# Performance work log

Measured on AMD Instinct MI355X. Metric: run time of the kernel, lower is better.

The kernel has to match this reference:

```python
import jax, jax.numpy as jnp
import numpy as np

D_MODEL = 2048
NUM_HEADS = 16
D_K = D_MODEL // NUM_HEADS
LORA_R = 8
LORA_ALPHA = 16
SCALING = LORA_ALPHA / LORA_R  # 2.0
B, S = 2, 2048


def setup_inputs() -> dict:
    key = jax.random.key(0)
    ks = jax.random.split(key, 17)
    s = 1.0 / np.sqrt(D_MODEL)
    d = {"x": jax.random.normal(ks[0], (B, S, D_MODEL), jnp.float32)}
    i = 1
    for name in ("q", "k", "v", "o"):
        d[f"W{name}"] = jax.random.uniform(ks[i], (D_MODEL, D_MODEL), jnp.float32, -s, s); i += 1
        d[f"b{name}"] = jax.random.uniform(ks[i], (D_MODEL,), jnp.float32, -s, s); i += 1
        d[f"A{name}"] = jax.random.uniform(ks[i], (LORA_R, D_MODEL), jnp.float32, -s, s); i += 1
        # lora_B is zero-initialized in the module, but use small random so grads flow meaningfully
        d[f"B{name}"] = jax.random.normal(ks[i], (D_MODEL, LORA_R), jnp.float32) * 0.01; i += 1
    return d


def _lora_linear(x, W, b, A, Bm):
    # F.linear(x, W, b) + (x @ A.T @ B.T) * scaling
    return x @ W.T + b + ((x @ A.T) @ Bm.T) * SCALING


def reference(x, Wq, bq, Aq, Bq, Wk, bk, Ak, Bk, Wv, bv, Av, Bv, Wo, bo, Ao, Bo):
    batch = x.shape[0]
    q = _lora_linear(x, Wq, bq, Aq, Bq)
    k = _lora_linear(x, Wk, bk, Ak, Bk)
    v = _lora_linear(x, Wv, bv, Av, Bv)
    # [B, S, H, Dk] -> [B, H, S, Dk]
    q = q.reshape(batch, -1, NUM_HEADS, D_K).transpose(0, 2, 1, 3)
    k = k.reshape(batch, -1, NUM_HEADS, D_K).transpose(0, 2, 1, 3)
    v = v.reshape(batch, -1, NUM_HEADS, D_K).transpose(0, 2, 1, 3)
    scores = jnp.einsum("bhqd,bhkd->bhqk", q, k) / jnp.sqrt(jnp.float32(D_K))
    attn = jax.nn.softmax(scores, axis=-1)
    context = jnp.einsum("bhqk,bhkd->bhqd", attn, v)
    context = context.transpose(0, 2, 1, 3).reshape(batch, -1, D_MODEL)
    return _lora_linear(context, Wo, bo, Ao, Bo)
```

## Files before the change

### kernel.cpp

```cpp
#include <hip/hip_runtime.h>
#include <stdint.h>

typedef unsigned short u16;
typedef unsigned int   u32;
typedef __bf16  bf16x8 __attribute__((ext_vector_type(8)));
typedef float   f32x4  __attribute__((ext_vector_type(4)));

#define LORA_SCALE 2.0f
#define QSCALE 0.08838834764831845f
#define LOG2E  1.4426950408889634f
#define RESCALE_THR 8.0f

__device__ __forceinline__ u16 f2bf(float f){
  u32 u = __builtin_bit_cast(u32, f);
  u32 r = (u + 0x7fffu + ((u >> 16) & 1u)) >> 16;
  return (u16)r;
}
__device__ __forceinline__ float bf2f(u16 v){
  return __builtin_bit_cast(float, ((u32)v) << 16);
}
__device__ __forceinline__ u32 cvt_pk_bf16(float lo, float hi){
  u32 d;
  asm("v_cvt_pk_bf16_f32 %0, %1, %2" : "=v"(d) : "v"(lo), "v"(hi));
  return d;
}

typedef __attribute__((address_space(3))) u32 lds_u32_t;
typedef __attribute__((address_space(1))) const u32 g_u32_t;

__device__ __forceinline__ void gload16(const void* g, void* l){
  __builtin_amdgcn_global_load_lds((g_u32_t*)(unsigned long long)g,
                                   (lds_u32_t*)(u32)(unsigned long long)l,
                                   16, 0, 0);
}

__global__ __launch_bounds__(256) void cvt_w4(const float* __restrict__ W0,
    const float* __restrict__ W1, const float* __restrict__ W2,
    const float* __restrict__ W3, u16* __restrict__ wqkv, u16* __restrict__ wo){
  int sel = blockIdx.x >> 11;
  int inner = blockIdx.x & 2047;
  const float* src = sel==0 ? W0 : sel==1 ? W1 : sel==2 ? W2 : W3;
  u16* dst = sel<3 ? (wqkv + (size_t)sel*4194304) : wo;
  int i = (inner*256 + threadIdx.x) * 8;
  float4 a = *(const float4*)(src + i);
  float4 b = *(const float4*)(src + i + 4);
  u16 o[8] = {f2bf(a.x),f2bf(a.y),f2bf(a.z),f2bf(a.w),
              f2bf(b.x),f2bf(b.y),f2bf(b.z),f2bf(b.w)};
  *(uint4*)(dst + i) = *(const uint4*)o;
}

__global__ __launch_bounds__(256) void lora_x_fused(const float* __restrict__ x,
    const float* __restrict__ A0, const float* __restrict__ A1, const float* __restrict__ A2,
    float* __restrict__ xout, u16* __restrict__ xbf){
  int w = threadIdx.x >> 6, lane = threadIdx.x & 63;
  int m = blockIdx.x * 4 + w;
  float acc[3][8];
  #pragma unroll
  for (int g=0; g<3; ++g)
    #pragma unroll
    for (int r=0; r<8; ++r) acc[g][r] = 0.f;
  const float* As[3] = {A0, A1, A2};
  #pragma unroll 1
  for (int it=0; it<8; ++it){
    int k = it*256 + lane*4;
    float4 xv = *(const float4*)(x + (size_t)m*2048 + k);
    u16 o[4] = {f2bf(xv.x), f2bf(xv.y), f2bf(xv.z), f2bf(xv.w)};
    *(uint2*)(xbf + (size_t)m*2048 + k) = *(const uint2*)o;
    #pragma unroll
    for (int g=0; g<3; ++g){
      const float* Ag = As[g];
      #pragma unroll
      for (int r=0; r<8; ++r){
        float4 av = *(const float4*)(Ag + r*2048 + k);
        acc[g][r] += xv.x*av.x + xv.y*av.y + xv.z*av.z + xv.w*av.w;
      }
    }
  }
  #pragma unroll
  for (int g=0; g<3; ++g)
    #pragma unroll
    for (int r=0; r<8; ++r){
      float v = acc[g][r];
      #pragma unroll
      for (int off=32; off; off>>=1) v += __shfl_xor(v, off);
      if (lane == 0) xout[g*32768 + m*8 + r] = v;
    }
}

__global__ __launch_bounds__(256) void lora_xa_bf16(const u16* __restrict__ xin,
    const float* __restrict__ A0, float* __restrict__ xout){
  int w = threadIdx.x >> 6, lane = threadIdx.x & 63;
  int m = blockIdx.x * 4 + w;
  float acc[8];
  #pragma unroll
  for (int r=0; r<8; ++r) acc[r] = 0.f;
  #pragma unroll 1
  for (int it=0; it<8; ++it){
    int k = it*256 + lane*4;
    ushort4 u = *(const ushort4*)(xin + (size_t)m*2048 + k);
    float4 xv = {bf2f(u.x), bf2f(u.y), bf2f(u.z), bf2f(u.w)};
    #pragma unroll
    for (int r=0; r<8; ++r){
      float4 av = *(const float4*)(A0 + r*2048 + k);
      acc[r] += xv.x*av.x + xv.y*av.y + xv.z*av.z + xv.w*av.w;
    }
  }
  #pragma unroll
  for (int r=0; r<8; ++r){
    float v = acc[r];
    #pragma unroll
    for (int off=32; off; off>>=1) v += __shfl_xor(v, off);
    if (lane == 0) xout[m*8 + r] = v;
  }
}

__device__ __forceinline__ void gemm_core_pipe(
    const u16* __restrict__ Arow, const u16* __restrict__ Wrow,
    u16* lds, int tid, f32x4 acc[4][4]){
  const int Kd = 2048, NT = 64;
  int w = tid >> 6, lane = tid & 63;
  int l15 = lane & 15, l4 = lane >> 4;
  int wm = w >> 1, wn = w & 1;
  int d0 = tid*16,        r0 = d0>>6, c0 = ((((d0>>4)&3) ^ ((r0>>1)&3))<<3);
  int d1 = 4096 + tid*16, r1 = d1>>6, c1 = ((((d1>>4)&3) ^ ((r1>>1)&3))<<3);

  auto STAGE = [&](int t, int pb){
    int kt = t*32;
    char* LA = (char*)lds + pb*16384;
    char* LB = LA + 8192;
    gload16(Arow + (size_t)r0*Kd + kt + c0, LA + w*1024);
    gload16(Wrow + (size_t)r0*Kd + kt + c0, LB + w*1024);
    gload16(Arow + (size_t)r1*Kd + kt + c1, LA + 4096 + w*1024);
    gload16(Wrow + (size_t)r1*Kd + kt + c1, LB + 4096 + w*1024);
  };

  STAGE(0,0); STAGE(1,1);
  asm volatile("s_waitcnt vmcnt(4)" ::: "memory");
  __builtin_amdgcn_s_barrier();

  int pc = 0, pn = 2;
  #pragma unroll 1
  for (int t=0; t<NT; ++t){
    if (t < NT-2) STAGE(t+2, pn);
    const u16* LA = lds + pc*8192;
    const u16* LB = LA + 4096;
    bf16x8 af[4], bfv[4];
    #pragma unroll
    for (int mi=0; mi<4; mi++){
      int r = wm*64 + mi*16 + l15;
      af[mi] = *(const bf16x8*)(LA + r*32 + ((l4 ^ ((r>>1)&3))<<3));
    }
    #pragma unroll
    for (int ni=0; ni<4; ni++){
      int r = wn*64 + ni*16 + l15;
      bfv[ni] = *(const bf16x8*)(LB + r*32 + ((l4 ^ ((r>>1)&3))<<3));
    }
    __builtin_amdgcn_s_setprio(1);
    #pragma unroll
    for (int mi=0; mi<4; mi++)
      #pragma unroll
      for (int ni=0; ni<4; ni++)
        acc[mi][ni] = __builtin_amdgcn_mfma_f32_16x16x32_bf16(af[mi], bfv[ni], acc[mi][ni], 0, 0, 0);
    __builtin_amdgcn_s_setprio(0);
    if (t < NT-2){
      asm volatile("s_waitcnt vmcnt(4)" ::: "memory");
      __builtin_amdgcn_s_barrier();
    } else if (t == NT-2){
      asm volatile("s_waitcnt vmcnt(0)" ::: "memory");
      __builtin_amdgcn_s_barrier();
    }
    pc = pc==2 ? 0 : pc+1;
    pn = pn==2 ? 0 : pn+1;
  }
}

__global__ __launch_bounds__(256, 3) void gemm_qkv(
    const u16* __restrict__ A, const u16* __restrict__ W,
    const float* __restrict__ bq, const float* __restrict__ bk, const float* __restrict__ bv,
    const float* __restrict__ lBq, const float* __restrict__ lBk, const float* __restrict__ lBv,
    const float* __restrict__ xa, u16* __restrict__ Qb, u16* __restrict__ Kb, u16* __restrict__ Vb){
  const int Kd = 2048;
  __shared__ u16 lds3[3*8192];
  int tid = threadIdx.x, lane = tid & 63;
  int l15 = lane & 15, l4 = lane >> 4;
  int w = tid >> 6, wm = w >> 1, wn = w & 1;
  int n0g = blockIdx.x * 128, m0 = blockIdx.y * 128;
  int which = blockIdx.x >> 4;
  int n0 = n0g & 2047;
  const float* bias = which==0 ? bq : which==1 ? bk : bv;
  const float* lB   = which==0 ? lBq : which==1 ? lBk : lBv;
  const float* xs   = xa + which*32768;
  u16* outp         = which==0 ? Qb : which==1 ? Kb : Vb;
  int swz = (which <= 1);
  float oscale = (which == 0) ? QSCALE*LOG2E : 1.0f;
  f32x4 acc[4][4];
  #pragma unroll
  for (int mi=0; mi<4; mi++)
    #pragma unroll
    for (int ni=0; ni<4; ni++) acc[mi][ni] = (f32x4){0.f,0.f,0.f,0.f};

  gemm_core_pipe(A + (size_t)m0*Kd, W + (size_t)n0g*Kd, lds3, tid, acc);

  float bvv[4]; float4 lb0[4], lb1[4];
  #pragma unroll
  for (int ni=0; ni<4; ni++){
    int col = n0 + wn*64 + ni*16 + l15;
    bvv[ni] = bias[col];
    lb0[ni] = *(const float4*)(lB + col*8);
    lb1[ni] = *(const float4*)(lB + col*8 + 4);
  }
  #pragma unroll
  for (int mi=0; mi<4; mi++)
    #pragma unroll
    for (int j=0; j<4; j++){
      int r = m0 + wm*64 + mi*16 + l4*4 + j;
      float4 xv0 = *(const float4*)(xs + (size_t)r*8);
      float4 xv1 = *(const float4*)(xs + (size_t)r*8 + 4);
      #pragma unroll
      for (int ni=0; ni<4; ni++){
        int col = n0 + wn*64 + ni*16 + l15;
        float v = acc[mi][ni][j] + bvv[ni] + LORA_SCALE * (
            xv0.x*lb0[ni].x + xv0.y*lb0[ni].y + xv0.z*lb0[ni].z + xv0.w*lb0[ni].w +
            xv1.x*lb1[ni].x + xv1.y*lb1[ni].y + xv1.z*lb1[ni].z + xv1.w*lb1[ni].w);
        v *= oscale;
        int cs = swz ? (col ^ ((r & 7) << 3)) : col;
        outp[(size_t)r*2048 + cs] = f2bf(v);
      }
    }
}

__global__ __launch_bounds__(256, 3) void gemm_o(
    const u16* __restrict__ A, const u16* __restrict__ W,
    const float* __restrict__ bias, const float* __restrict__ lB,
    const float* __restrict__ xa, float* __restrict__ outp){
  const int Kd = 2048, Nd = 2048;
  __shared__ u16 lds3[3*8192];
  int tid = threadIdx.x, lane = tid & 63;
  int l15 = lane & 15, l4 = lane >> 4;
  int w = tid >> 6, wm = w >> 1, wn = w & 1;
  int n0 = blockIdx.x * 128, m0 = blockIdx.y * 128;
  f32x4 acc[4][4];
  #pragma unroll
  for (int mi=0; mi<4; mi++)
    #pragma unroll
    for (int ni=0; ni<4; ni++) acc[mi][ni] = (f32x4){0.f,0.f,0.f,0.f};

  gemm_core_pipe(A + (size_t)m0*Kd, W + (size_t)n0*Kd, lds3, tid, acc);

  float bv[4]; float4 lb0[4], lb1[4];
  #pragma unroll
  for (int ni=0; ni<4; ni++){
    int col = n0 + wn*64 + ni*16 + l15;
    bv[ni] = bias[col];
    lb0[ni] = *(const float4*)(lB + col*8);
    lb1[ni] = *(const float4*)(lB + col*8 + 4);
  }
  #pragma unroll
  for (int mi=0; mi<4; mi++)
    #pragma unroll
    for (int j=0; j<4; j++){
      int r = m0 + wm*64 + mi*16 + l4*4 + j;
      float4 xv0 = *(const float4*)(xa + (size_t)r*8);
      float4 xv1 = *(const float4*)(xa + (size_t)r*8 + 4);
      #pragma unroll
      for (int ni=0; ni<4; ni++){
        int col = n0 + wn*64 + ni*16 + l15;
        float v = acc[mi][ni][j] + bv[ni] + LORA_SCALE * (
            xv0.x*lb0[ni].x + xv0.y*lb0[ni].y + xv0.z*lb0[ni].z + xv0.w*lb0[ni].w +
            xv1.x*lb1[ni].x + xv1.y*lb1[ni].y + xv1.z*lb1[ni].z + xv1.w*lb1[ni].w);
        outp[(size_t)r*Nd + col] = v;
      }
    }
}

__global__ __launch_bounds__(256) void transpose_v(const u16* __restrict__ V,
                                                   u16* __restrict__ Vt){
  __shared__ u16 tile[64*80];
  int tid = threadIdx.x;
  int f0 = blockIdx.x * 64, m0 = blockIdx.y * 64;
  int i = tid >> 2, j0 = (tid & 3) * 16;
  #pragma unroll
  for (int kk=0; kk<16; kk+=8){
    uint4 u = *(const uint4*)(V + (size_t)(m0 + i)*2048 + f0 + j0 + kk);
    *(uint4*)(tile + i*80 + j0 + kk) = u;
  }
  __syncthreads();
  int j = tid >> 2, i0 = (tid & 3) * 16;
  int b = m0 >> 11, s0 = m0 & 2047;
  int h = f0 >> 7, d = (f0 & 127) + j;
  int c = (d & 7) << 3;
  size_t obase = ((size_t)((b*16 + h)*128 + d)) * 2048 + s0;
  #pragma unroll
  for (int kk=0; kk<16; kk+=8){
    u16 v8[8];
    #pragma unroll
    for (int u2=0; u2<8; ++u2) v8[u2] = tile[(i0+kk+u2)*80 + j];
    *(uint4*)(Vt + obase + ((i0+kk) ^ c)) = *(const uint4*)v8;
  }
}

__global__ __launch_bounds__(256, 2) void attn_kernel(
    const u16* __restrict__ Q, const u16* __restrict__ K,
    const u16* __restrict__ Vt, u16* __restrict__ ctx){
  __shared__ u16 buf[2][16384];
  __shared__ u16 Psh[4*32*64];
  int tid = threadIdx.x, w = tid >> 6, lane = tid & 63;
  int l15 = lane & 15, l4 = lane >> 4;
  int lin = blockIdx.x;
  int virt = (lin & 7) * 64 + (lin >> 3);
  int qt = virt & 15, bh = virt >> 4;
  int b = bh >> 4, h = bh & 15;
  const u16* Qg = Q + (size_t)(b*2048 + qt*128) * 2048 + h*128;
  const u16* Kg = K + (size_t)(b*2048) * 2048 + h*128;
  const u16* Vg = Vt + (size_t)bh * 128 * 2048;

  #pragma unroll
  for (int i=0; i<8; ++i){
    int e = (i*256 + tid) * 8;
    int r = e >> 7, cc = e & 127;
    gload16(Qg + (size_t)r*2048 + cc, (char*)buf[1] + i*4096 + w*1024);
  }
  #pragma unroll
  for (int i=0; i<4; ++i){
    int e = (i*256 + tid) * 8;
    int r = e >> 7, cc = e & 127;
    gload16(Kg + (size_t)r*2048 + cc, (char*)buf[0] + i*4096 + w*1024);
    int dd = e >> 6, c2 = e & 63;
    gload16(Vg + (size_t)dd*2048 + c2, (char*)buf[0] + 16384 + i*4096 + w*1024);
  }
  __syncthreads();

  bf16x8 qf[2][4];
  #pragma unroll
  for (int mi=0; mi<2; mi++){
    int r = w*32 + mi*16 + l15;
    #pragma unroll
    for (int kb=0; kb<4; kb++){
      int cc = (kb*32 + l4*8) ^ ((r & 7) << 3);
      qf[mi][kb] = *(const bf16x8*)(buf[1] + r*128 + cc);
    }
  }
  __syncthreads();

  f32x4 ctxa[2][8];
  #pragma unroll
  for (int mi=0; mi<2; mi++)
    #pragma unroll
    for (int nd=0; nd<8; nd++) ctxa[mi][nd] = (f32x4){0.f,0.f,0.f,0.f};
  float mrun[2] = {-3.0e38f, -3.0e38f};
  float lrun[2] = {0.f, 0.f};

  char* PwB = (char*)(Psh + w * (32*64));
  int psw = (l15 & 7) << 4;

  for (int t = 0; t < 32; ++t){
    int cur = t & 1;
    const u16* Kc = buf[cur];
    const u16* Vc = buf[cur] + 8192;
    if (t + 1 < 32){
      int kvn = (t + 1) * 64;
      char* bn = (char*)buf[cur ^ 1];
      #pragma unroll
      for (int i=0; i<4; ++i){
        int e = (i*256 + tid) * 8;
        int r = e >> 7, cc = e & 127;
        gload16(Kg + (size_t)(kvn + r)*2048 + cc, bn + i*4096 + w*1024);
        int dd = e >> 6, c2 = e & 63;
        gload16(Vg + (size_t)dd*2048 + kvn + c2, bn + 16384 + i*4096 + w*1024);
      }
    }
    f32x4 s[2][4];
    #pragma unroll
    for (int mi=0; mi<2; mi++)
      #pragma unroll
      for (int ni=0; ni<4; ni++) s[mi][ni] = (f32x4){0.f,0.f,0.f,0.f};
    __builtin_amdgcn_s_setprio(1);
    #pragma unroll
    for (int kb=0; kb<4; kb++){
      #pragma unroll
      for (int ni=0; ni<4; ni++){
        int r = ni*16 + l15;
        int cc = (kb*32 + l4*8) ^ ((r & 7) << 3);
        bf16x8 kf = *(const bf16x8*)(Kc + r*128 + cc);
        s[0][ni] = __builtin_amdgcn_mfma_f32_16x16x32_bf16(kf, qf[0][kb], s[0][ni], 0, 0, 0);
        s[1][ni] = __builtin_amdgcn_mfma_f32_16x16x32_bf16(kf, qf[1][kb], s[1][ni], 0, 0, 0);
      }
    }
    __builtin_amdgcn_s_setprio(0);
    float pm[2];
    #pragma unroll
    for (int mi=0; mi<2; mi++){
      float v = s[mi][0][0];
      #pragma unroll
      for (int ni=0; ni<4; ni++)
        #pragma unroll
        for (int j=0; j<4; j++) v = fmaxf(v, s[mi][ni][j]);
      v = fmaxf(v, __shfl_xor(v, 16));
      v = fmaxf(v, __shfl_xor(v, 32));
      pm[mi] = v;
    }
    bool need = (pm[0] > mrun[0] + RESCALE_THR) || (pm[1] > mrun[1] + RESCALE_THR);
    if (__any(need)){
      #pragma unroll
      for (int mi=0; mi<2; mi++){
        float mnew = fmaxf(mrun[mi], pm[mi]);
        float cr = exp2f(mrun[mi] - mnew);
        lrun[mi] *= cr;
        mrun[mi] = mnew;
        #pragma unroll
        for (int nd=0; nd<8; nd++) ctxa[mi][nd] *= cr;
      }
    }
    #pragma unroll
    for (int mi=0; mi<2; mi++){
      float ps = 0.f;
      #pragma unroll
      for (int ni=0; ni<4; ni++){
        float p0 = exp2f(s[mi][ni][0] - mrun[mi]);
        float p1 = exp2f(s[mi][ni][1] - mrun[mi]);
        float p2 = exp2f(s[mi][ni][2] - mrun[mi]);
        float p3 = exp2f(s[mi][ni][3] - mrun[mi]);
        ps += (p0 + p1) + (p2 + p3);
        uint2 pk = {cvt_pk_bf16(p0, p1), cvt_pk_bf16(p2, p3)};
        *(uint2*)(PwB + (mi*16 + l15)*128 + ((ni*32 + l4*8) ^ psw)) = pk;
      }
      ps += __shfl_xor(ps, 16);
      ps += __shfl_xor(ps, 32);
      lrun[mi] += ps;
    }
    bf16x8 pb[2][2];
    #pragma unroll
    for (int mi=0; mi<2; mi++)
      #pragma unroll
      for (int kvb=0; kvb<2; kvb++)
        pb[mi][kvb] = *(const bf16x8*)(PwB + (mi*16 + l15)*128 + ((kvb*64 + l4*16) ^ psw));
    __builtin_amdgcn_s_setprio(1);
    #pragma unroll
    for (int nd=0; nd<8; nd++){
      int dd = nd*16 + l15;
      int sw = (dd & 7) << 3;
      #pragma unroll
      for (int kvb=0; kvb<2; kvb++){
        bf16x8 vf = *(const bf16x8*)(Vc + dd*64 + ((kvb*32 + l4*8) ^ sw));
        ctxa[0][nd] = __builtin_amdgcn_mfma_f32_16x16x32_bf16(vf, pb[0][kvb], ctxa[0][nd], 0, 0, 0);
        ctxa[1][nd] = __builtin_amdgcn_mfma_f32_16x16x32_bf16(vf, pb[1][kvb], ctxa[1][nd], 0, 0, 0);
      }
    }
    __builtin_amdgcn_s_setprio(0);
    __syncthreads();
  }
  char* OwB = (char*)buf[0] + w*8192;
  #pragma unroll
  for (int mi=0; mi<2; mi++){
    float inv = 1.0f / lrun[mi];
    #pragma unroll
    for (int nd=0; nd<8; nd++){
      f32x4 c = ctxa[mi][nd] * inv;
      uint2 pk = {cvt_pk_bf16(c[0], c[1]), cvt_pk_bf16(c[2], c[3])};
      *(uint2*)(OwB + (mi*16 + l15)*256 + ((nd*32 + l4*8) ^ psw)) = pk;
    }
  }
  #pragma unroll
  for (int i=0; i<8; ++i){
    int row = i*4 + l4;
    int colb = l15*16;
    uint4 v = *(const uint4*)(OwB + row*256 + (colb ^ ((row & 7) << 4)));
    int srow = qt*128 + w*32 + row;
    *(uint4*)(ctx + ((size_t)(b*2048 + srow))*2048 + h*128 + colb/2) = v;
  }
}

extern "C" void kernel_launch(void* const* d_in, const int* in_sizes, int n_in,
                              void* d_out, int out_size, void* d_ws, size_t ws_size,
                              hipStream_t stream){
  const float* x  = (const float*)d_in[0];
  const float* Wq = (const float*)d_in[1];  const float* bq = (const float*)d_in[2];
  const float* Aq = (const float*)d_in[3];  const float* Bq = (const float*)d_in[4];
  const float* Wk = (const float*)d_in[5];  const float* bk = (const float*)d_in[6];
  const float* Ak = (const float*)d_in[7];  const float* Bk = (const float*)d_in[8];
  const float* Wv = (const float*)d_in[9];  const float* bv = (const float*)d_in[10];
  const float* Av = (const float*)d_in[11]; const float* Bv = (const float*)d_in[12];
  const float* Wo = (const float*)d_in[13]; const float* bo = (const float*)d_in[14];
  const float* Ao = (const float*)d_in[15]; const float* Bo = (const float*)d_in[16];

  char* ws = (char*)d_ws;
  size_t off = 0;
  u16* xbf  = (u16*)(ws + off); off += (size_t)4096*2048*2;
  u16* wqkv = (u16*)(ws + off); off += (size_t)3*2048*2048*2;
  u16* wob  = (u16*)(ws + off); off += (size_t)2048*2048*2;
  float* xa = (float*)(ws + off); off += (size_t)4*32768*4;
  u16* Qb  = (u16*)(ws + off); off += (size_t)4096*2048*2;
  u16* Kb  = (u16*)(ws + off); off += (size_t)4096*2048*2;
  u16* Vb  = (u16*)(ws + off); off += (size_t)4096*2048*2;
  u16* Vtb = (u16*)(ws + off); off += (size_t)4096*2048*2;
  if (ws_size < off) return;

  cvt_w4<<<8192, 256, 0, stream>>>(Wq, Wk, Wv, Wo, wqkv, wob);
  lora_x_fused<<<1024, 256, 0, stream>>>(x, Aq, Ak, Av, xa, xbf);

  gemm_qkv<<<dim3(48,32), 256, 0, stream>>>(xbf, wqkv, bq, bk, bv, Bq, Bk, Bv, xa, Qb, Kb, Vb);

  transpose_v<<<dim3(32,64), 256, 0, stream>>>(Vb, Vtb);

  attn_kernel<<<512, 256, 0, stream>>>(Qb, Kb, Vtb, Vb);

  lora_xa_bf16<<<1024, 256, 0, stream>>>(Vb, Ao, xa+98304);

  gemm_o<<<dim3(16,32), 256, 0, stream>>>(Vb, wob, bo, Bo, xa+98304, (float*)d_out);
}
```

Baseline: 357.2 us.

## Use 256x128 GEMM tiles with 8 waves, 4-stage LDS ring, and XCD-aware block remap

Replaces the 128x128, 4-wave GEMM core with a 256x128 tile computed by 8 waves (512 threads). Each wave does half its MFMAs per phase, interleaving A and B prefetches three stages ahead in a 4-buffer LDS ring with extra barriers. Blocks are remapped to a 1D grid so consecutive blocks on the same XCD share tiles. The goal is more operand reuse per byte loaded and better L2 locality, at the cost of larger LDS use (96KB), more barriers per iteration, and fewer blocks, which may leave CUs under-filled.

New measurement: 355.0 us. Within noise of the previous version (-0.6%).

```diff
diff --git a/kernel.cpp b/kernel.cpp
--- a/kernel.cpp
+++ b/kernel.cpp
@@ -114,114 +114,130 @@
   }
 }
 
-__device__ __forceinline__ void gemm_core_pipe(
-    const u16* __restrict__ Arow, const u16* __restrict__ Wrow,
+__device__ __forceinline__ void gemm_core_256(
+    const u16* __restrict__ Aptr,
+    const u16* __restrict__ Wptr,
     u16* lds, int tid, f32x4 acc[4][4]){
-  const int Kd = 2048, NT = 64;
-  int w = tid >> 6, lane = tid & 63;
-  int l15 = lane & 15, l4 = lane >> 4;
+  const int Kd = 2048;
+  int l = tid & 63, w = tid >> 6;
+  int l15 = l & 15, l4 = l >> 4;
   int wm = w >> 1, wn = w & 1;
-  int d0 = tid*16,        r0 = d0>>6, c0 = ((((d0>>4)&3) ^ ((r0>>1)&3))<<3);
-  int d1 = 4096 + tid*16, r1 = d1>>6, c1 = ((((d1>>4)&3) ^ ((r1>>1)&3))<<3);
-
-  auto STAGE = [&](int t, int pb){
-    int kt = t*32;
-    char* LA = (char*)lds + pb*16384;
-    char* LB = LA + 8192;
-    gload16(Arow + (size_t)r0*Kd + kt + c0, LA + w*1024);
-    gload16(Wrow + (size_t)r0*Kd + kt + c0, LB + w*1024);
-    gload16(Arow + (size_t)r1*Kd + kt + c1, LA + 4096 + w*1024);
-    gload16(Wrow + (size_t)r1*Kd + kt + c1, LB + 4096 + w*1024);
-  };
-
-  STAGE(0,0); STAGE(1,1);
-  asm volatile("s_waitcnt vmcnt(4)" ::: "memory");
+  int srow = w*16 + (l >> 2);
+  int scol = ((l & 3) ^ ((l >> 3) & 3)) * 8;
+  const u16* asrc0 = Aptr + (size_t)srow * Kd + scol;
+  const u16* asrc1 = asrc0 + (size_t)128 * Kd;
+  const u16* bsrc  = Wptr + (size_t)srow * Kd + scol;
+  char* L = (char*)lds;
+  int wb = w * 1024;
+
+  int rsw = ((l4 ^ ((l15 >> 1) & 3)) << 4);
+  int abase = (wm*64 + l15)*64 + rsw;
+  int bbase = 16384 + (wn*64 + l15)*64 + rsw;
+
+  #define STAGE_A(t) { int bb_ = ((t)&3)*24576; \
+      gload16(asrc0 + (t)*32, L + bb_ + wb); \
+      gload16(asrc1 + (t)*32, L + bb_ + 8192 + wb); }
+  #define STAGE_B(t) { int bb_ = ((t)&3)*24576; \
+      gload16(bsrc + (t)*32, L + bb_ + 16384 + wb); }
+
+  STAGE_A(0); STAGE_B(0); STAGE_A(1); STAGE_B(1); STAGE_A(2); STAGE_B(2);
+  asm volatile("s_waitcnt vmcnt(6)" ::: "memory");
   __builtin_amdgcn_s_barrier();
 
-  int pc = 0, pn = 2;
   #pragma unroll 1
-  for (int t=0; t<NT; ++t){
-    if (t < NT-2) STAGE(t+2, pn);
-    const u16* LA = lds + pc*8192;
-    const u16* LB = LA + 4096;
-    bf16x8 af[4], bfv[4];
-    #pragma unroll
-    for (int mi=0; mi<4; mi++){
-      int r = wm*64 + mi*16 + l15;
-      af[mi] = *(const bf16x8*)(LA + r*32 + ((l4 ^ ((r>>1)&3))<<3));
-    }
-    #pragma unroll
-    for (int ni=0; ni<4; ni++){
-      int r = wn*64 + ni*16 + l15;
-      bfv[ni] = *(const bf16x8*)(LB + r*32 + ((l4 ^ ((r>>1)&3))<<3));
-    }
+  for (int t = 0; t < 64; ++t){
+    int bb = (t & 3) * 24576;
+    bf16x8 bf[4], af0, af1;
+    af0 = *(const bf16x8*)(L + bb + abase);
+    af1 = *(const bf16x8*)(L + bb + abase + 1024);
+    #pragma unroll
+    for (int nr=0; nr<4; ++nr) bf[nr] = *(const bf16x8*)(L + bb + bbase + nr*1024);
+    if (t < 61) STAGE_A(t+3);
+    __builtin_amdgcn_s_barrier();
     __builtin_amdgcn_s_setprio(1);
     #pragma unroll
-    for (int mi=0; mi<4; mi++)
-      #pragma unroll
-      for (int ni=0; ni<4; ni++)
-        acc[mi][ni] = __builtin_amdgcn_mfma_f32_16x16x32_bf16(af[mi], bfv[ni], acc[mi][ni], 0, 0, 0);
+    for (int nr=0; nr<4; ++nr){
+      acc[0][nr] = __builtin_amdgcn_mfma_f32_16x16x32_bf16(af0, bf[nr], acc[0][nr], 0, 0, 0);
+      acc[1][nr] = __builtin_amdgcn_mfma_f32_16x16x32_bf16(af1, bf[nr], acc[1][nr], 0, 0, 0);
+    }
     __builtin_amdgcn_s_setprio(0);
-    if (t < NT-2){
-      asm volatile("s_waitcnt vmcnt(4)" ::: "memory");
-      __builtin_amdgcn_s_barrier();
-    } else if (t == NT-2){
+    __builtin_amdgcn_s_barrier();
+    af0 = *(const bf16x8*)(L + bb + abase + 2048);
+    af1 = *(const bf16x8*)(L + bb + abase + 3072);
+    if (t < 61){
+      STAGE_B(t+3);
+      asm volatile("s_waitcnt vmcnt(6)" ::: "memory");
+    } else if (t == 61){
+      asm volatile("s_waitcnt vmcnt(3)" ::: "memory");
+    } else if (t == 62){
       asm volatile("s_waitcnt vmcnt(0)" ::: "memory");
-      __builtin_amdgcn_s_barrier();
-    }
-    pc = pc==2 ? 0 : pc+1;
-    pn = pn==2 ? 0 : pn+1;
-  }
-}
-
-__global__ __launch_bounds__(256, 3) void gemm_qkv(
+    }
+    __builtin_amdgcn_s_barrier();
+    __builtin_amdgcn_s_setprio(1);
+    #pragma unroll
+    for (int nr=0; nr<4; ++nr){
+      acc[2][nr] = __builtin_amdgcn_mfma_f32_16x16x32_bf16(af0, bf[nr], acc[2][nr], 0, 0, 0);
+      acc[3][nr] = __builtin_amdgcn_mfma_f32_16x16x32_bf16(af1, bf[nr], acc[3][nr], 0, 0, 0);
+    }
+    __builtin_amdgcn_s_setprio(0);
+    __builtin_amdgcn_s_barrier();
+  }
+  #undef STAGE_A
+  #undef STAGE_B
+}
+
+__global__ __launch_bounds__(512, 2) void gemm_qkv(
     const u16* __restrict__ A, const u16* __restrict__ W,
     const float* __restrict__ bq, const float* __restrict__ bk, const float* __restrict__ bv,
     const float* __restrict__ lBq, const float* __restrict__ lBk, const float* __restrict__ lBv,
     const float* __restrict__ xa, u16* __restrict__ Qb, u16* __restrict__ Kb, u16* __restrict__ Vb){
-  const int Kd = 2048;
-  __shared__ u16 lds3[3*8192];
-  int tid = threadIdx.x, lane = tid & 63;
-  int l15 = lane & 15, l4 = lane >> 4;
-  int w = tid >> 6, wm = w >> 1, wn = w & 1;
-  int n0g = blockIdx.x * 128, m0 = blockIdx.y * 128;
-  int which = blockIdx.x >> 4;
-  int n0 = n0g & 2047;
+  __shared__ u16 lds[49152];
+  int tid = threadIdx.x;
+  int l = tid & 63, w = tid >> 6;
+  int l15 = l & 15, l4 = l >> 4;
+  int wm = w >> 1, wn = w & 1;
+  int bid = blockIdx.x;
+  int virt = (bid & 7) * 96 + (bid >> 3);
+  int mt = virt & 15, nt = virt >> 4;
+  int m0 = mt * 256, n0g = nt * 128;
+  int which = nt >> 4;
+  int n0 = (nt & 15) * 128;
   const float* bias = which==0 ? bq : which==1 ? bk : bv;
   const float* lB   = which==0 ? lBq : which==1 ? lBk : lBv;
   const float* xs   = xa + which*32768;
   u16* outp         = which==0 ? Qb : which==1 ? Kb : Vb;
   int swz = (which <= 1);
   float oscale = (which == 0) ? QSCALE*LOG2E : 1.0f;
+
   f32x4 acc[4][4];
   #pragma unroll
-  for (int mi=0; mi<4; mi++)
-    #pragma unroll
-    for (int ni=0; ni<4; ni++) acc[mi][ni] = (f32x4){0.f,0.f,0.f,0.f};
-
-  gemm_core_pipe(A + (size_t)m0*Kd, W + (size_t)n0g*Kd, lds3, tid, acc);
+  for (int mr=0; mr<4; mr++)
+    #pragma unroll
+    for (int nr=0; nr<4; nr++) acc[mr][nr] = (f32x4){0.f,0.f,0.f,0.f};
+
+  gemm_core_256(A + (size_t)m0*2048, W + (size_t)n0g*2048, lds, tid, acc);
 
   float bvv[4]; float4 lb0[4], lb1[4];
   #pragma unroll
-  for (int ni=0; ni<4; ni++){
-    int col = n0 + wn*64 + ni*16 + l15;
-    bvv[ni] = bias[col];
-    lb0[ni] = *(const float4*)(lB + col*8);
-    lb1[ni] = *(const float4*)(lB + col*8 + 4);
-  }
-  #pragma unroll
-  for (int mi=0; mi<4; mi++)
+  for (int nr=0; nr<4; nr++){
+    int col = n0 + wn*64 + nr*16 + l15;
+    bvv[nr] = bias[col];
+    lb0[nr] = *(const float4*)(lB + col*8);
+    lb1[nr] = *(const float4*)(lB + col*8 + 4);
+  }
+  #pragma unroll
+  for (int mr=0; mr<4; mr++)
     #pragma unroll
     for (int j=0; j<4; j++){
-      int r = m0 + wm*64 + mi*16 + l4*4 + j;
+      int r = m0 + wm*64 + mr*16 + l4*4 + j;
       float4 xv0 = *(const float4*)(xs + (size_t)r*8);
       float4 xv1 = *(const float4*)(xs + (size_t)r*8 + 4);
       #pragma unroll
-      for (int ni=0; ni<4; ni++){
-        int col = n0 + wn*64 + ni*16 + l15;
-        float v = acc[mi][ni][j] + bvv[ni] + LORA_SCALE * (
-            xv0.x*lb0[ni].x + xv0.y*lb0[ni].y + xv0.z*lb0[ni].z + xv0.w*lb0[ni].w +
-            xv1.x*lb1[ni].x + xv1.y*lb1[ni].y + xv1.z*lb1[ni].z + xv1.w*lb1[ni].w);
+      for (int nr=0; nr<4; nr++){
+        int col = n0 + wn*64 + nr*16 + l15;
+        float v = acc[mr][nr][j] + bvv[nr] + LORA_SCALE * (
+            xv0.x*lb0[nr].x + xv0.y*lb0[nr].y + xv0.z*lb0[nr].z + xv0.w*lb0[nr].w +
+            xv1.x*lb1[nr].x + xv1.y*lb1[nr].y + xv1.z*lb1[nr].z + xv1.w*lb1[nr].w);
         v *= oscale;
         int cs = swz ? (col ^ ((r & 7) << 3)) : col;
         outp[(size_t)r*2048 + cs] = f2bf(v);
@@ -229,46 +245,50 @@
     }
 }
 
-__global__ __launch_bounds__(256, 3) void gemm_o(
+__global__ __launch_bounds__(512, 2) void gemm_o(
     const u16* __restrict__ A, const u16* __restrict__ W,
     const float* __restrict__ bias, const float* __restrict__ lB,
     const float* __restrict__ xa, float* __restrict__ outp){
-  const int Kd = 2048, Nd = 2048;
-  __shared__ u16 lds3[3*8192];
-  int tid = threadIdx.x, lane = tid & 63;
-  int l15 = lane & 15, l4 = lane >> 4;
-  int w = tid >> 6, wm = w >> 1, wn = w & 1;
-  int n0 = blockIdx.x * 128, m0 = blockIdx.y * 128;
+  __shared__ u16 lds[49152];
+  int tid = threadIdx.x;
+  int l = tid & 63, w = tid >> 6;
+  int l15 = l & 15, l4 = l >> 4;
+  int wm = w >> 1, wn = w & 1;
+  int bid = blockIdx.x;
+  int virt = (bid & 7) * 32 + (bid >> 3);
+  int mt = virt & 15, nt = virt >> 4;
+  int m0 = mt * 256, n0 = nt * 128;
+
   f32x4 acc[4][4];
   #pragma unroll
-  for (int mi=0; mi<4; mi++)
-    #pragma unroll
-    for (int ni=0; ni<4; ni++) acc[mi][ni] = (f32x4){0.f,0.f,0.f,0.f};
-
-  gemm_core_pipe(A + (size_t)m0*Kd, W + (size_t)n0*Kd, lds3, tid, acc);
+  for (int mr=0; mr<4; mr++)
+    #pragma unroll
+    for (int nr=0; nr<4; nr++) acc[mr][nr] = (f32x4){0.f,0.f,0.f,0.f};
+
+  gemm_core_256(A + (size_t)m0*2048, W + (size_t)n0*2048, lds, tid, acc);
 
   float bv[4]; float4 lb0[4], lb1[4];
   #pragma unroll
-  for (int ni=0; ni<4; ni++){
-    int col = n0 + wn*64 + ni*16 + l15;
-    bv[ni] = bias[col];
-    lb0[ni] = *(const float4*)(lB + col*8);
-    lb1[ni] = *(const float4*)(lB + col*8 + 4);
-  }
-  #pragma unroll
-  for (int mi=0; mi<4; mi++)
+  for (int nr=0; nr<4; nr++){
+    int col = n0 + wn*64 + nr*16 + l15;
+    bv[nr] = bias[col];
+    lb0[nr] = *(const float4*)(lB + col*8);
+    lb1[nr] = *(const float4*)(lB + col*8 + 4);
+  }
+  #pragma unroll
+  for (int mr=0; mr<4; mr++)
     #pragma unroll
     for (int j=0; j<4; j++){
-      int r = m0 + wm*64 + mi*16 + l4*4 + j;
+      int r = m0 + wm*64 + mr*16 + l4*4 + j;
       float4 xv0 = *(const float4*)(xa + (size_t)r*8);
       float4 xv1 = *(const float4*)(xa + (size_t)r*8 + 4);
       #pragma unroll
-      for (int ni=0; ni<4; ni++){
-        int col = n0 + wn*64 + ni*16 + l15;
-        float v = acc[mi][ni][j] + bv[ni] + LORA_SCALE * (
-            xv0.x*lb0[ni].x + xv0.y*lb0[ni].y + xv0.z*lb0[ni].z + xv0.w*lb0[ni].w +
-            xv1.x*lb1[ni].x + xv1.y*lb1[ni].y + xv1.z*lb1[ni].z + xv1.w*lb1[ni].w);
-        outp[(size_t)r*Nd + col] = v;
+      for (int nr=0; nr<4; nr++){
+        int col = n0 + wn*64 + nr*16 + l15;
+        float v = acc[mr][nr][j] + bv[nr] + LORA_SCALE * (
+            xv0.x*lb0[nr].x + xv0.y*lb0[nr].y + xv0.z*lb0[nr].z + xv0.w*lb0[nr].w +
+            xv1.x*lb1[nr].x + xv1.y*lb1[nr].y + xv1.z*lb1[nr].z + xv1.w*lb1[nr].w);
+        outp[(size_t)r*2048 + col] = v;
       }
     }
 }
@@ -498,7 +518,7 @@
   cvt_w4<<<8192, 256, 0, stream>>>(Wq, Wk, Wv, Wo, wqkv, wob);
   lora_x_fused<<<1024, 256, 0, stream>>>(x, Aq, Ak, Av, xa, xbf);
 
-  gemm_qkv<<<dim3(48,32), 256, 0, stream>>>(xbf, wqkv, bq, bk, bv, Bq, Bk, Bv, xa, Qb, Kb, Vb);
+  gemm_qkv<<<768, 512, 0, stream>>>(xbf, wqkv, bq, bk, bv, Bq, Bk, Bv, xa, Qb, Kb, Vb);
 
   transpose_v<<<dim3(32,64), 256, 0, stream>>>(Vb, Vtb);
 
@@ -506,5 +526,5 @@
 
   lora_xa_bf16<<<1024, 256, 0, stream>>>(Vb, Ao, xa+98304);
 
-  gemm_o<<<dim3(16,32), 256, 0, stream>>>(Vb, wob, bo, Bo, xa+98304, (float*)d_out);
-}
+  gemm_o<<<256, 512, 0, stream>>>(Vb, wob, bo, Bo, xa+98304, (float*)d_out);
+}
```
